# Performance work log

Measured on AMD Instinct MI355X. Metric: run time of the kernel, lower is better.

Reference implementation:

```python
import jax, jax.numpy as jnp
import numpy as np
from jax import lax

B, T, D_IN, D_PROJ, D_OUT, LORDER = 16, 2048, 1024, 512, 1024, 20


def setup_inputs() -> dict:
    key = jax.random.key(0)
    k1, k2, k3, k4 = jax.random.split(key, 4)
    s = 0.05
    return {
        "input": jax.random.normal(k1, (B, T, D_IN), dtype=jnp.float32),
        "in_cache": jnp.zeros((B, D_PROJ, LORDER - 1), dtype=jnp.float32),
        "W_lin": jax.random.normal(k2, (D_IN, D_PROJ), dtype=jnp.float32) * s,
        "conv_w": jax.random.normal(k3, (D_PROJ, LORDER), dtype=jnp.float32) * s,
        "W_aff": jax.random.normal(k4, (D_PROJ, D_OUT), dtype=jnp.float32) * s,
        "b_aff": jnp.zeros((D_OUT,), dtype=jnp.float32),
    }


def reference(input, in_cache, W_lin, conv_w, W_aff, b_aff):
    L = conv_w.shape[1]
    # 1) linear down-projection (no bias): [B,T,Din] -> [B,T,Dp]
    x = jnp.einsum("btd,dp->btp", input, W_lin)
    # 2) FSMN causal depthwise memory block with streaming cache
    xt = jnp.swapaxes(x, 1, 2)                       # [B,Dp,T]
    cat = jnp.concatenate([in_cache, xt], axis=2)    # [B,Dp,T+L-1]
    out_cache = cat[:, :, -(L - 1):]                 # last L-1 frames for next chunk
    # depthwise conv over time, VALID padding -> output length T
    y = lax.conv_general_dilated(
        cat, conv_w[:, None, :],                      # rhs [Dp,1,L]
        window_strides=(1,), padding="VALID",
        dimension_numbers=("NCH", "OIH", "NCH"),
        feature_group_count=conv_w.shape[0])
    m = jnp.swapaxes(y + xt, 1, 2)                   # residual add, back to [B,T,Dp]
    # 3) affine up-projection + 4) ReLU
    out = jax.nn.relu(jnp.einsum("btp,po->bto", m, W_aff) + b_aff)
    return (out, out_cache)
```

## Files before the change

kernel.cpp:

```cpp
#include <hip/hip_runtime.h>
#include <cstdint>
#include <cstddef>

#define B_  16
#define T_  2048
#define DIN 1024
#define DPJ 512
#define DOUT 1024
#define LORD 20
#define HALO (LORD - 1)
#define M_ROWS (B_ * T_)
#define OUT0_ELEMS ((size_t)M_ROWS * DOUT)
#define CACHE_ELEMS ((size_t)B_ * DPJ * (LORD - 1))

typedef __bf16 bf16_t;
typedef __bf16 bf16x2 __attribute__((ext_vector_type(2)));
typedef __bf16 bf16x4 __attribute__((ext_vector_type(4)));
typedef __bf16 bf16x8 __attribute__((ext_vector_type(8)));
typedef float  f32x4  __attribute__((ext_vector_type(4)));

__device__ __forceinline__ void async_load16(const void* g, void* lds_base) {
    __builtin_amdgcn_global_load_lds(
        (const __attribute__((address_space(1))) unsigned int*)g,
        (__attribute__((address_space(3))) unsigned int*)lds_base,
        16, 0, 0);
}

__device__ __forceinline__ int xcd_swizzle(int hw, int nwg) {
    int cpx = nwg >> 3;
    return (hw & 7) * cpx + (hw >> 3);
}

__global__ __launch_bounds__(256) void prep_weights(
    const float* __restrict__ Wl, const float* __restrict__ Wa,
    bf16_t* __restrict__ WlT, bf16_t* __restrict__ WaT) {
    int idx = blockIdx.x * 256 + threadIdx.x;
    const int n1 = DIN * DPJ;
    if (idx < n1) {
        int k = idx / DPJ, n = idx - k * DPJ;
        WlT[(size_t)n * DIN + k] = (bf16_t)Wl[idx];
    } else {
        int j = idx - n1;
        if (j < DPJ * DOUT) {
            int k = j / DOUT, n = j - k * DOUT;
            WaT[(size_t)n * DPJ + k] = (bf16_t)Wa[j];
        }
    }
}

__global__ __launch_bounds__(256) void gemm1_fused(
    const float* __restrict__ A, const bf16_t* __restrict__ Bt,
    bf16_t* __restrict__ C, const int M, const int N, const int K) {
    __shared__ bf16_t sA[128 * 64];
    __shared__ bf16_t sB[128 * 64];

    const int tid  = threadIdx.x;
    const int lane = tid & 63;
    const int wave = tid >> 6;

    const int gx   = gridDim.x;
    const int hw   = blockIdx.y * gx + blockIdx.x;
    const int lid  = xcd_swizzle(hw, gx * gridDim.y);
    const int lby  = lid / gx;
    const int lbx  = lid - lby * gx;
    const int col0 = lbx * 128;
    const int row0 = lby * 128;

    const int s4   = tid & 3;
    const int arow = tid >> 2;
    const float* gA = A + (size_t)(row0 + arow) * K + s4 * 8;
    const int o0 = ((s4       ^ (arow & 7)) << 3);
    const int o1 = (((s4 + 4) ^ (arow & 7)) << 3);
    bf16_t* dst0 = sA + arow * 64;
    bf16_t* dst1 = sA + (arow + 64) * 64;

    const int lr  = lane >> 3;
    const int jsw = (lane & 7) ^ lr;
    const bf16_t* gB0 = Bt + (size_t)(col0 + wave * 32 + lr) * K + jsw * 8;
    bf16_t* lB0 = sB + wave * 2048;

    const int wm = (wave >> 1) * 64;
    const int wn = (wave & 1) * 64;
    const int fr = lane & 15;
    const int fk = lane >> 4;

    const f32x4 zero = {0.f, 0.f, 0.f, 0.f};
    f32x4 acc[4][4];
#pragma unroll
    for (int mt = 0; mt < 4; ++mt)
#pragma unroll
        for (int nt = 0; nt < 4; ++nt) acc[mt][nt] = zero;

    for (int k0 = 0; k0 < K; k0 += 64) {
        __syncthreads();

        f32x4 g0a = *(const f32x4*)(gA + k0);
        f32x4 g0b = *(const f32x4*)(gA + k0 + 4);
        f32x4 g0c = *(const f32x4*)(gA + k0 + 32);
        f32x4 g0d = *(const f32x4*)(gA + k0 + 36);
        f32x4 g1a = *(const f32x4*)(gA + (size_t)64 * K + k0);
        f32x4 g1b = *(const f32x4*)(gA + (size_t)64 * K + k0 + 4);
        f32x4 g1c = *(const f32x4*)(gA + (size_t)64 * K + k0 + 32);
        f32x4 g1d = *(const f32x4*)(gA + (size_t)64 * K + k0 + 36);

#pragma unroll
        for (int c = 0; c < 4; ++c)
            async_load16(gB0 + (size_t)c * 8 * K + k0, lB0 + c * 512);

        {
            bf16x8 v0 = { (bf16_t)g0a[0], (bf16_t)g0a[1], (bf16_t)g0a[2], (bf16_t)g0a[3],
                          (bf16_t)g0b[0], (bf16_t)g0b[1], (bf16_t)g0b[2], (bf16_t)g0b[3] };
            bf16x8 v1 = { (bf16_t)g0c[0], (bf16_t)g0c[1], (bf16_t)g0c[2], (bf16_t)g0c[3],
                          (bf16_t)g0d[0], (bf16_t)g0d[1], (bf16_t)g0d[2], (bf16_t)g0d[3] };
            *(bf16x8*)(dst0 + o0) = v0;
            *(bf16x8*)(dst0 + o1) = v1;
            bf16x8 w0 = { (bf16_t)g1a[0], (bf16_t)g1a[1], (bf16_t)g1a[2], (bf16_t)g1a[3],
                          (bf16_t)g1b[0], (bf16_t)g1b[1], (bf16_t)g1b[2], (bf16_t)g1b[3] };
            bf16x8 w1 = { (bf16_t)g1c[0], (bf16_t)g1c[1], (bf16_t)g1c[2], (bf16_t)g1c[3],
                          (bf16_t)g1d[0], (bf16_t)g1d[1], (bf16_t)g1d[2], (bf16_t)g1d[3] };
            *(bf16x8*)(dst1 + o0) = w0;
            *(bf16x8*)(dst1 + o1) = w1;
        }

        __syncthreads();

#pragma unroll
        for (int h = 0; h < 2; ++h) {
            bf16x8 af[4], bfr[4];
#pragma unroll
            for (int mt = 0; mt < 4; ++mt) {
                int r = wm + mt * 16 + fr;
                int j = h * 4 + fk;
                af[mt] = *(const bf16x8*)(sA + r * 64 + ((j ^ (r & 7)) << 3));
            }
#pragma unroll
            for (int nt = 0; nt < 4; ++nt) {
                int r = wn + nt * 16 + fr;
                int j = h * 4 + fk;
                bfr[nt] = *(const bf16x8*)(sB + r * 64 + ((j ^ (r & 7)) << 3));
            }
#pragma unroll
            for (int mt = 0; mt < 4; ++mt)
#pragma unroll
                for (int nt = 0; nt < 4; ++nt)
                    acc[mt][nt] = __builtin_amdgcn_mfma_f32_16x16x32_bf16(
                        af[mt], bfr[nt], acc[mt][nt], 0, 0, 0);
        }
    }

    const int er = row0 + wm + (lane >> 4) * 4;
    const int ec = col0 + wn + (lane & 15);
#pragma unroll
    for (int mt = 0; mt < 4; ++mt)
#pragma unroll
        for (int nt = 0; nt < 4; ++nt)
#pragma unroll
            for (int rr = 0; rr < 4; ++rr)
                C[(size_t)(er + mt * 16 + rr) * N + (ec + nt * 16)] =
                    (bf16_t)acc[mt][nt][rr];
}

__global__ __launch_bounds__(256) void gemm_bt_relu(
    const bf16_t* __restrict__ A, const bf16_t* __restrict__ Bt,
    float* __restrict__ C, const float* __restrict__ bias,
    const int M, const int N, const int K) {
    __shared__ bf16_t sA[128 * 64];
    __shared__ bf16_t sB[128 * 64];

    const int tid  = threadIdx.x;
    const int lane = tid & 63;
    const int wave = tid >> 6;

    const int gx   = gridDim.x;
    const int hw   = blockIdx.y * gx + blockIdx.x;
    const int lid  = xcd_swizzle(hw, gx * gridDim.y);
    const int lby  = lid / gx;
    const int lbx  = lid - lby * gx;
    const int col0 = lbx * 128;
    const int row0 = lby * 128;

    const int lr   = lane >> 3;
    const int jsw  = (lane & 7) ^ lr;
    const bf16_t* gA0 = A  + (size_t)(row0 + wave * 32 + lr) * K + jsw * 8;
    const bf16_t* gB0 = Bt + (size_t)(col0 + wave * 32 + lr) * K + jsw * 8;
    bf16_t* lA0 = sA + wave * 2048;
    bf16_t* lB0 = sB + wave * 2048;

    const int wm = (wave >> 1) * 64;
    const int wn = (wave & 1) * 64;
    const int fr = lane & 15;
    const int fk = lane >> 4;

    const f32x4 zero = {0.f, 0.f, 0.f, 0.f};
    f32x4 acc[4][4];
#pragma unroll
    for (int mt = 0; mt < 4; ++mt)
#pragma unroll
        for (int nt = 0; nt < 4; ++nt) acc[mt][nt] = zero;

    for (int k0 = 0; k0 < K; k0 += 64) {
        __syncthreads();
#pragma unroll
        for (int c = 0; c < 4; ++c) {
            async_load16(gA0 + (size_t)c * 8 * K + k0, lA0 + c * 512);
            async_load16(gB0 + (size_t)c * 8 * K + k0, lB0 + c * 512);
        }
        __syncthreads();

#pragma unroll
        for (int h = 0; h < 2; ++h) {
            bf16x8 af[4], bfr[4];
#pragma unroll
            for (int mt = 0; mt < 4; ++mt) {
                int r = wm + mt * 16 + fr;
                int j = h * 4 + fk;
                af[mt] = *(const bf16x8*)(sA + r * 64 + ((j ^ (r & 7)) << 3));
            }
#pragma unroll
            for (int nt = 0; nt < 4; ++nt) {
                int r = wn + nt * 16 + fr;
                int j = h * 4 + fk;
                bfr[nt] = *(const bf16x8*)(sB + r * 64 + ((j ^ (r & 7)) << 3));
            }
#pragma unroll
            for (int mt = 0; mt < 4; ++mt)
#pragma unroll
                for (int nt = 0; nt < 4; ++nt)
                    acc[mt][nt] = __builtin_amdgcn_mfma_f32_16x16x32_bf16(
                        af[mt], bfr[nt], acc[mt][nt], 0, 0, 0);
        }
    }

    const int er = row0 + wm + (lane >> 4) * 4;
    const int ec = col0 + wn + (lane & 15);
#pragma unroll
    for (int nt = 0; nt < 4; ++nt) {
        float bb = bias[ec + nt * 16];
#pragma unroll
        for (int mt = 0; mt < 4; ++mt)
#pragma unroll
            for (int rr = 0; rr < 4; ++rr) {
                float v = acc[mt][nt][rr] + bb;
                C[(size_t)(er + mt * 16 + rr) * N + (ec + nt * 16)] =
                    v > 0.f ? v : 0.f;
            }
    }
}

#define TT 64
#define PPT 128
__global__ __launch_bounds__(256) void dwconv_tiled(
    const bf16_t* __restrict__ x, const float* __restrict__ cache,
    const float* __restrict__ cw, bf16_t* __restrict__ m,
    float* __restrict__ oc) {
    __shared__ float sx[(TT + HALO) * PPT];

    const int tid = threadIdx.x;
    const int t0  = blockIdx.x * TT;
    const int b   = blockIdx.y;
    const int p0  = blockIdx.z * PPT;

    for (int c = tid; c < (TT + HALO) * PPT / 8; c += 256) {
        int r    = c >> 4;
        int col  = (c & 15) << 3;
        int trow = t0 - HALO + r;
        float* dst = sx + r * PPT + col;
        if (trow >= 0) {
            bf16x8 v = *(const bf16x8*)(x + ((size_t)(b * T_ + trow)) * DPJ + p0 + col);
#pragma unroll
            for (int i = 0; i < 8; ++i) dst[i] = (float)v[i];
        } else {
#pragma unroll
            for (int i = 0; i < 8; ++i)
                dst[i] = cache[((size_t)b * DPJ + p0 + col + i) * HALO + (trow + HALO)];
        }
    }
    __syncthreads();

    const int pp   = tid & 63;
    const int half = tid >> 6;
    const int tb   = half * 16;
    const float2* sx2 = (const float2*)sx;

    const int pg = p0 + 2 * pp;
    float2 w[LORD];
#pragma unroll
    for (int l = 0; l < LORD; ++l) {
        w[l].x = cw[pg * LORD + l];
        w[l].y = cw[(pg + 1) * LORD + l];
    }

    float2 win[LORD];
#pragma unroll
    for (int i = 0; i < HALO; ++i) win[i] = sx2[(tb + i) * 64 + pp];

#pragma unroll
    for (int tl = 0; tl < 16; ++tl) {
        float2 nv = sx2[(tb + tl + HALO) * 64 + pp];
        win[(tl + HALO) % LORD] = nv;
        float2 s = nv;
#pragma unroll
        for (int l = 0; l < LORD; ++l) {
            float2 v = win[(tl + l) % LORD];
            s.x += w[l].x * v.x;
            s.y += w[l].y * v.y;
        }
        bf16x2 o = { (bf16_t)s.x, (bf16_t)s.y };
        *(bf16x2*)(m + ((size_t)(b * T_ + t0 + tb + tl)) * DPJ + pg) = o;
    }

    if (blockIdx.x == (T_ / TT) - 1) {
        for (int i = tid; i < PPT * HALO; i += 256) {
            int pl = i / HALO;
            int j  = i - pl * HALO;
            oc[((size_t)b * DPJ + p0 + pl) * HALO + j] = sx[(64 + j) * PPT + pl];
        }
    }
}

extern "C" void kernel_launch(void* const* d_in, const int* in_sizes, int n_in,
                              void* d_out, int out_size, void* d_ws, size_t ws_size,
                              hipStream_t stream) {
    const float* input    = (const float*)d_in[0];
    const float* in_cache = (const float*)d_in[1];
    const float* W_lin    = (const float*)d_in[2];
    const float* conv_w   = (const float*)d_in[3];
    const float* W_aff    = (const float*)d_in[4];
    const float* b_aff    = (const float*)d_in[5];
    float* out = (float*)d_out;

    char* ws = (char*)d_ws;
    bf16_t* x_buf = (bf16_t*)(ws);
    bf16_t* m_buf = (bf16_t*)(ws + 33554432);
    bf16_t* WlinT = (bf16_t*)(ws + 67108864);
    bf16_t* WaffT = (bf16_t*)(ws + 67108864 + 1048576);

    prep_weights<<<(DIN * DPJ + DPJ * DOUT + 255) / 256, 256, 0, stream>>>(
        W_lin, W_aff, WlinT, WaffT);

    gemm1_fused<<<dim3(DPJ / 128, M_ROWS / 128), 256, 0, stream>>>(
        input, WlinT, x_buf, M_ROWS, DPJ, DIN);

    dwconv_tiled<<<dim3(T_ / TT, B_, DPJ / PPT), 256, 0, stream>>>(
        x_buf, in_cache, conv_w, m_buf, out + OUT0_ELEMS);

    gemm_bt_relu<<<dim3(DOUT / 128, M_ROWS / 128), 256, 0, stream>>>(
        m_buf, WaffT, out, b_aff, M_ROWS, DOUT, DPJ);
}
```

Before: 349.9 us.

## Use 512-thread blocks in both GEMMs and register-prefetch A tiles in gemm1

Both GEMM kernels now run with 8 waves per block instead of 4, with each wave computing a 64x32 sub-tile, which halves per-thread accumulators and loads. The aim is more latency hiding through higher wave counts. gemm1 also loads the next k-step's fp32 A tile into registers ahead of time and uses explicit waitcnt and barriers in place of __syncthreads. The risk is more LDS fragment reads per MFMA and brittle hand-placed wait counts.

```diff
diff --git a/kernel.cpp b/kernel.cpp
--- a/kernel.cpp
+++ b/kernel.cpp
@@ -48,7 +48,7 @@
     }
 }
 
-__global__ __launch_bounds__(256) void gemm1_fused(
+__global__ __launch_bounds__(512, 4) void gemm1_fused(
     const float* __restrict__ A, const bf16_t* __restrict__ Bt,
     bf16_t* __restrict__ C, const int M, const int N, const int K) {
     __shared__ bf16_t sA[128 * 64];
@@ -72,39 +72,38 @@
     const int o0 = ((s4       ^ (arow & 7)) << 3);
     const int o1 = (((s4 + 4) ^ (arow & 7)) << 3);
     bf16_t* dst0 = sA + arow * 64;
-    bf16_t* dst1 = sA + (arow + 64) * 64;
 
     const int lr  = lane >> 3;
     const int jsw = (lane & 7) ^ lr;
-    const bf16_t* gB0 = Bt + (size_t)(col0 + wave * 32 + lr) * K + jsw * 8;
-    bf16_t* lB0 = sB + wave * 2048;
-
-    const int wm = (wave >> 1) * 64;
-    const int wn = (wave & 1) * 64;
+    const bf16_t* gB0 = Bt + (size_t)(col0 + wave * 16 + lr) * K + jsw * 8;
+    bf16_t* lB0 = sB + wave * 1024;
+
+    const int wm = (wave >> 2) * 64;
+    const int wn = (wave & 3) * 32;
     const int fr = lane & 15;
     const int fk = lane >> 4;
 
     const f32x4 zero = {0.f, 0.f, 0.f, 0.f};
-    f32x4 acc[4][4];
+    f32x4 acc[4][2];
 #pragma unroll
     for (int mt = 0; mt < 4; ++mt)
 #pragma unroll
-        for (int nt = 0; nt < 4; ++nt) acc[mt][nt] = zero;
+        for (int nt = 0; nt < 2; ++nt) acc[mt][nt] = zero;
+
+    f32x4 g0a, g0b, g0c, g0d;
+    g0a = *(const f32x4*)(gA);
+    g0b = *(const f32x4*)(gA + 4);
+    g0c = *(const f32x4*)(gA + 32);
+    g0d = *(const f32x4*)(gA + 36);
 
     for (int k0 = 0; k0 < K; k0 += 64) {
-        __syncthreads();
-
-        f32x4 g0a = *(const f32x4*)(gA + k0);
-        f32x4 g0b = *(const f32x4*)(gA + k0 + 4);
-        f32x4 g0c = *(const f32x4*)(gA + k0 + 32);
-        f32x4 g0d = *(const f32x4*)(gA + k0 + 36);
-        f32x4 g1a = *(const f32x4*)(gA + (size_t)64 * K + k0);
-        f32x4 g1b = *(const f32x4*)(gA + (size_t)64 * K + k0 + 4);
-        f32x4 g1c = *(const f32x4*)(gA + (size_t)64 * K + k0 + 32);
-        f32x4 g1d = *(const f32x4*)(gA + (size_t)64 * K + k0 + 36);
-
-#pragma unroll
-        for (int c = 0; c < 4; ++c)
+        asm volatile("s_waitcnt lgkmcnt(0)" ::: "memory");
+        __builtin_amdgcn_sched_barrier(0);
+        __builtin_amdgcn_s_barrier();
+        __builtin_amdgcn_sched_barrier(0);
+
+#pragma unroll
+        for (int c = 0; c < 2; ++c)
             async_load16(gB0 + (size_t)c * 8 * K + k0, lB0 + c * 512);
 
         {
@@ -114,19 +113,25 @@
                           (bf16_t)g0d[0], (bf16_t)g0d[1], (bf16_t)g0d[2], (bf16_t)g0d[3] };
             *(bf16x8*)(dst0 + o0) = v0;
             *(bf16x8*)(dst0 + o1) = v1;
-            bf16x8 w0 = { (bf16_t)g1a[0], (bf16_t)g1a[1], (bf16_t)g1a[2], (bf16_t)g1a[3],
-                          (bf16_t)g1b[0], (bf16_t)g1b[1], (bf16_t)g1b[2], (bf16_t)g1b[3] };
-            bf16x8 w1 = { (bf16_t)g1c[0], (bf16_t)g1c[1], (bf16_t)g1c[2], (bf16_t)g1c[3],
-                          (bf16_t)g1d[0], (bf16_t)g1d[1], (bf16_t)g1d[2], (bf16_t)g1d[3] };
-            *(bf16x8*)(dst1 + o0) = w0;
-            *(bf16x8*)(dst1 + o1) = w1;
-        }
-
-        __syncthreads();
+        }
+
+        const int kn = k0 + 64;
+        if (kn < K) {
+            g0a = *(const f32x4*)(gA + kn);
+            g0b = *(const f32x4*)(gA + kn + 4);
+            g0c = *(const f32x4*)(gA + kn + 32);
+            g0d = *(const f32x4*)(gA + kn + 36);
+            asm volatile("s_waitcnt vmcnt(4) lgkmcnt(0)" ::: "memory");
+        } else {
+            asm volatile("s_waitcnt vmcnt(0) lgkmcnt(0)" ::: "memory");
+        }
+        __builtin_amdgcn_sched_barrier(0);
+        __builtin_amdgcn_s_barrier();
+        __builtin_amdgcn_sched_barrier(0);
 
 #pragma unroll
         for (int h = 0; h < 2; ++h) {
-            bf16x8 af[4], bfr[4];
+            bf16x8 af[4], bfr[2];
 #pragma unroll
             for (int mt = 0; mt < 4; ++mt) {
                 int r = wm + mt * 16 + fr;
@@ -134,7 +139,7 @@
                 af[mt] = *(const bf16x8*)(sA + r * 64 + ((j ^ (r & 7)) << 3));
             }
 #pragma unroll
-            for (int nt = 0; nt < 4; ++nt) {
+            for (int nt = 0; nt < 2; ++nt) {
                 int r = wn + nt * 16 + fr;
                 int j = h * 4 + fk;
                 bfr[nt] = *(const bf16x8*)(sB + r * 64 + ((j ^ (r & 7)) << 3));
@@ -142,7 +147,7 @@
 #pragma unroll
             for (int mt = 0; mt < 4; ++mt)
 #pragma unroll
-                for (int nt = 0; nt < 4; ++nt)
+                for (int nt = 0; nt < 2; ++nt)
                     acc[mt][nt] = __builtin_amdgcn_mfma_f32_16x16x32_bf16(
                         af[mt], bfr[nt], acc[mt][nt], 0, 0, 0);
         }
@@ -153,14 +158,14 @@
 #pragma unroll
     for (int mt = 0; mt < 4; ++mt)
 #pragma unroll
-        for (int nt = 0; nt < 4; ++nt)
+        for (int nt = 0; nt < 2; ++nt)
 #pragma unroll
             for (int rr = 0; rr < 4; ++rr)
                 C[(size_t)(er + mt * 16 + rr) * N + (ec + nt * 16)] =
                     (bf16_t)acc[mt][nt][rr];
 }
 
-__global__ __launch_bounds__(256) void gemm_bt_relu(
+__global__ __launch_bounds__(512, 4) void gemm_bt_relu(
     const bf16_t* __restrict__ A, const bf16_t* __restrict__ Bt,
     float* __restrict__ C, const float* __restrict__ bias,
     const int M, const int N, const int K) {
@@ -181,27 +186,27 @@
 
     const int lr   = lane >> 3;
     const int jsw  = (lane & 7) ^ lr;
-    const bf16_t* gA0 = A  + (size_t)(row0 + wave * 32 + lr) * K + jsw * 8;
-    const bf16_t* gB0 = Bt + (size_t)(col0 + wave * 32 + lr) * K + jsw * 8;
-    bf16_t* lA0 = sA + wave * 2048;
-    bf16_t* lB0 = sB + wave * 2048;
-
-    const int wm = (wave >> 1) * 64;
-    const int wn = (wave & 1) * 64;
+    const bf16_t* gA0 = A  + (size_t)(row0 + wave * 16 + lr) * K + jsw * 8;
+    const bf16_t* gB0 = Bt + (size_t)(col0 + wave * 16 + lr) * K + jsw * 8;
+    bf16_t* lA0 = sA + wave * 1024;
+    bf16_t* lB0 = sB + wave * 1024;
+
+    const int wm = (wave >> 2) * 64;
+    const int wn = (wave & 3) * 32;
     const int fr = lane & 15;
     const int fk = lane >> 4;
 
     const f32x4 zero = {0.f, 0.f, 0.f, 0.f};
-    f32x4 acc[4][4];
+    f32x4 acc[4][2];
 #pragma unroll
     for (int mt = 0; mt < 4; ++mt)
 #pragma unroll
-        for (int nt = 0; nt < 4; ++nt) acc[mt][nt] = zero;
+        for (int nt = 0; nt < 2; ++nt) acc[mt][nt] = zero;
 
     for (int k0 = 0; k0 < K; k0 += 64) {
         __syncthreads();
 #pragma unroll
-        for (int c = 0; c < 4; ++c) {
+        for (int c = 0; c < 2; ++c) {
             async_load16(gA0 + (size_t)c * 8 * K + k0, lA0 + c * 512);
             async_load16(gB0 + (size_t)c * 8 * K + k0, lB0 + c * 512);
         }
@@ -209,7 +214,7 @@
 
 #pragma unroll
         for (int h = 0; h < 2; ++h) {
-            bf16x8 af[4], bfr[4];
+            bf16x8 af[4], bfr[2];
 #pragma unroll
             for (int mt = 0; mt < 4; ++mt) {
                 int r = wm + mt * 16 + fr;
@@ -217,7 +222,7 @@
                 af[mt] = *(const bf16x8*)(sA + r * 64 + ((j ^ (r & 7)) << 3));
             }
 #pragma unroll
-            for (int nt = 0; nt < 4; ++nt) {
+            for (int nt = 0; nt < 2; ++nt) {
                 int r = wn + nt * 16 + fr;
                 int j = h * 4 + fk;
                 bfr[nt] = *(const bf16x8*)(sB + r * 64 + ((j ^ (r & 7)) << 3));
@@ -225,7 +230,7 @@
 #pragma unroll
             for (int mt = 0; mt < 4; ++mt)
 #pragma unroll
-                for (int nt = 0; nt < 4; ++nt)
+                for (int nt = 0; nt < 2; ++nt)
                     acc[mt][nt] = __builtin_amdgcn_mfma_f32_16x16x32_bf16(
                         af[mt], bfr[nt], acc[mt][nt], 0, 0, 0);
         }
@@ -234,7 +239,7 @@
     const int er = row0 + wm + (lane >> 4) * 4;
     const int ec = col0 + wn + (lane & 15);
 #pragma unroll
-    for (int nt = 0; nt < 4; ++nt) {
+    for (int nt = 0; nt < 2; ++nt) {
         float bb = bias[ec + nt * 16];
 #pragma unroll
         for (int mt = 0; mt < 4; ++mt)
@@ -338,12 +343,12 @@
     prep_weights<<<(DIN * DPJ + DPJ * DOUT + 255) / 256, 256, 0, stream>>>(
         W_lin, W_aff, WlinT, WaffT);
 
-    gemm1_fused<<<dim3(DPJ / 128, M_ROWS / 128), 256, 0, stream>>>(
+    gemm1_fused<<<dim3(DPJ / 128, M_ROWS / 128), 512, 0, stream>>>(
         input, WlinT, x_buf, M_ROWS, DPJ, DIN);
 
     dwconv_tiled<<<dim3(T_ / TT, B_, DPJ / PPT), 256, 0, stream>>>(
         x_buf, in_cache, conv_w, m_buf, out + OUT0_ELEMS);
 
-    gemm_bt_relu<<<dim3(DOUT / 128, M_ROWS / 128), 256, 0, stream>>>(
+    gemm_bt_relu<<<dim3(DOUT / 128, M_ROWS / 128), 512, 0, stream>>>(
         m_buf, WaffT, out, b_aff, M_ROWS, DOUT, DPJ);
 }
```

After: 363.8 us. +4.0%, slower.
